# Kernel tuning notes

Hardware: AMD Instinct MI355X
Metric: run time of the kernel (lower is better)

## Reference

```python
import jax, jax.numpy as jnp
import numpy as np

B = 1      # batch
D = 64     # octree grid side at this level
N = 65536  # active voxels
C = 32     # channels (nin == nout for resblock)
K = 3      # kernel size


def _offsets():
    r = jnp.arange(K) - K // 2
    oz, oy, ox = jnp.meshgrid(r, r, r, indexing='ij')
    return jnp.stack([oz.ravel(), oy.ravel(), ox.ravel()], axis=-1)  # [27,3] (kz,ky,kx order)


def octree_conv3d(values, indices, mask_values, kernel, bias, activation=None):
    # values: [N,Cin], indices: [N,4] (b,z,y,x), mask_values: [N,1]
    Cin = values.shape[-1]
    Cout = kernel.shape[-1]
    taps = kernel.reshape(K * K * K, Cin, Cout)            # kz,ky,kx order == kernel[kz,ky,kx]
    vals = jnp.einsum('nc,tcd->tnd', values, taps)         # [27,N,Cout]
    offs = _offsets()                                      # [27,3]
    coords = indices[:, 1:]                                # [N,3]
    # shift = [0, kz-1, ky-1, kx-1]; clamp to [0, D-1] (stride=inv_stride=1)
    sh = jnp.clip(coords[None, :, :] + offs[:, None, :], 0, D - 1)  # [27,N,3]
    lin = indices[:, 0][None, :] * (D * D * D) + sh[..., 0] * (D * D) + sh[..., 1] * D + sh[..., 2]
    grid = jnp.zeros((B * D * D * D, Cout), dtype=values.dtype)
    grid = grid.at[lin.reshape(-1)].add(vals.reshape(-1, Cout))     # scatter-add == coalesce sum
    out_lin = indices[:, 0] * (D * D * D) + coords[:, 0] * (D * D) + coords[:, 1] * D + coords[:, 2]
    gathered = grid[out_lin]                               # [N,Cout] values at mask positions
    out = (gathered + mask_values * bias[None, :]) * mask_values     # result + mask*bias; result*mask
    if activation is not None:
        out = activation(out)
    return out


def setup_inputs() -> dict:
    key = jax.random.key(0)
    k1, k2, k3, k4, k5, k6 = jax.random.split(key, 6)
    G = B * D * D * D
    perm = jax.random.permutation(k1, G)[:N]               # unique (coalesced) voxel indices
    b = perm // (D * D * D)
    rem = perm % (D * D * D)
    z = rem // (D * D)
    y = (rem // D) % D
    x = rem % D
    indices = jnp.stack([b, z, y, x], axis=-1).astype(jnp.int64)   # [N,4]
    values = jax.random.normal(k2, (N, C), dtype=jnp.float32)
    mask_values = jnp.ones((N, 1), dtype=jnp.float32)
    stdv = 1.0 / np.sqrt(K * K * K * C)
    kern1 = (jax.random.uniform(k3, (K, K, K, C, C)) - 0.5) * 2.0 * stdv
    bias1 = (jax.random.uniform(k4, (C,)) - 0.5) * 2.0 * stdv
    kern2 = (jax.random.uniform(k5, (K, K, K, C, C)) - 0.5) * 2.0 * stdv
    bias2 = (jax.random.uniform(k6, (C,)) - 0.5) * 2.0 * stdv
    return {'values': values, 'indices': indices, 'mask_values': mask_values,
            'kern1': kern1, 'bias1': bias1, 'kern2': kern2, 'bias2': bias2}


def reference(values, indices, mask_values, kern1, bias1, kern2, bias2):
    # OctreeResblock: conv(relu) -> conv -> residual add, all on the sparse index set
    h = octree_conv3d(values, indices, mask_values, kern1, bias1, activation=jax.nn.relu)
    h = octree_conv3d(h, indices, mask_values, kern2, bias2, activation=None)
    return values + h
```

## Files before the change

### kernel.cpp

```cpp
#include <hip/hip_runtime.h>

#define NPTS 65536
#define CCH  32
#define DDIM 64
#define GVOX (DDIM*DDIM*DDIM)
#define MAXTILES 4128

typedef _Float16 half8  __attribute__((ext_vector_type(8)));
typedef _Float16 half4v __attribute__((ext_vector_type(4)));
typedef float    floatx4 __attribute__((ext_vector_type(4)));

__global__ __launch_bounds__(256) void k_prep0(
    int* __restrict__ map, int* __restrict__ sorted,
    const float* __restrict__ values, _Float16* __restrict__ valsh,
    const float* __restrict__ k1, const float* __restrict__ k2,
    _Float16* __restrict__ w1, _Float16* __restrict__ w2,
    _Float16* __restrict__ hh, int* __restrict__ pcoord,
    int* __restrict__ cnt, int* __restrict__ slot)
{
  int tid = blockIdx.x * 256 + threadIdx.x;
  if (tid < GVOX/4) { ((int4*)map)[tid] = make_int4(-1,-1,-1,-1); return; }
  tid -= GVOX/4;
  if (tid < MAXTILES*16) { sorted[tid] = NPTS; return; }
  tid -= MAXTILES*16;
  if (tid < (NPTS*CCH)/4) {
    float4 v = ((const float4*)values)[tid];
    half4v h = { (_Float16)v.x, (_Float16)v.y, (_Float16)v.z, (_Float16)v.w };
    ((half4v*)valsh)[tid] = h; return;
  }
  tid -= (NPTS*CCH)/4;
  if (tid < 27*CCH*CCH) {
    int t = tid/(CCH*CCH), r = tid%(CCH*CCH);
    int cin = r/CCH, cout = r%CCH;
    int o = (t*CCH + cout)*CCH + cin;
    w1[o] = (_Float16)k1[tid]; w2[o] = (_Float16)k2[tid]; return;
  }
  tid -= 27*CCH*CCH;
  if (tid < CCH) { valsh[NPTS*CCH+tid] = (_Float16)0.f; hh[NPTS*CCH+tid] = (_Float16)0.f; return; }
  tid -= CCH;
  if (tid < 27) { cnt[tid] = 0; slot[tid] = 0; return; }
  tid -= 27;
  if (tid == 0) pcoord[NPTS] = 0;
}
#define PREP0_THREADS (GVOX/4 + MAXTILES*16 + (NPTS*CCH)/4 + 27*CCH*CCH + CCH + 27 + 1)

__global__ __launch_bounds__(256) void k_prep1(const int* __restrict__ idx,
                                               int* __restrict__ map,
                                               int* __restrict__ pcoord,
                                               int* __restrict__ cls,
                                               int* __restrict__ cnt)
{
  __shared__ int lcnt[27];
  if (threadIdx.x < 27) lcnt[threadIdx.x] = 0;
  __syncthreads();
  const int n = blockIdx.x*256 + threadIdx.x;
  const int b = idx[4*n], z = idx[4*n+1], y = idx[4*n+2], x = idx[4*n+3];
  map[((b*DDIM + z)*DDIM + y)*DDIM + x] = n;
  pcoord[n] = (b<<18) | (z<<12) | (y<<6) | x;
  const int cz = (z==0)?0:((z==DDIM-1)?2:1);
  const int cy = (y==0)?0:((y==DDIM-1)?2:1);
  const int cx = (x==0)?0:((x==DDIM-1)?2:1);
  const int c = cz*9 + cy*3 + cx;
  cls[n] = c;
  atomicAdd(&lcnt[c], 1);
  __syncthreads();
  if (threadIdx.x < 27 && lcnt[threadIdx.x]) atomicAdd(&cnt[threadIdx.x], lcnt[threadIdx.x]);
}

__global__ void k_prep2(const int* __restrict__ cnt, int* __restrict__ clsbase,
                        int* __restrict__ tstart, int* __restrict__ ntiles)
{
  if (threadIdx.x == 0 && blockIdx.x == 0) {
    int b = 0, tb = 0;
    for (int c = 0; c < 27; ++c) {
      clsbase[c] = b; tstart[c] = tb;
      int nt = (cnt[c] + 15) >> 4;
      b += nt << 4; tb += nt;
    }
    tstart[27] = tb; *ntiles = tb;
  }
}

__global__ __launch_bounds__(256) void k_prep3(const int* __restrict__ cls,
                                               const int* __restrict__ clsbase,
                                               int* __restrict__ slot,
                                               int* __restrict__ sorted,
                                               const int* __restrict__ tstart,
                                               const int* __restrict__ ntp,
                                               int* __restrict__ tileclass)
{
  if (blockIdx.x < NPTS/256) {
    __shared__ int lcnt[27], lbase[27];
    if (threadIdx.x < 27) lcnt[threadIdx.x] = 0;
    __syncthreads();
    const int n = blockIdx.x*256 + threadIdx.x;
    const int c = cls[n];
    const int lrank = atomicAdd(&lcnt[c], 1);
    __syncthreads();
    if (threadIdx.x < 27)
      lbase[threadIdx.x] = lcnt[threadIdx.x] ? atomicAdd(&slot[threadIdx.x], lcnt[threadIdx.x]) : 0;
    __syncthreads();
    sorted[clsbase[c] + lbase[c] + lrank] = n;
  } else {
    const int i = (blockIdx.x - NPTS/256)*256 + threadIdx.x;
    if (i >= MAXTILES) return;
    const int nt = *ntp;
    int c = 13;
    if (i < nt) {
      for (int cc = 0; cc < 27; ++cc)
        if (i >= tstart[cc] && i < tstart[cc+1]) { c = cc; break; }
    }
    tileclass[i] = c;
  }
}

template<int MODE>
__global__ __launch_bounds__(256) void conv_mfma(
    const _Float16* __restrict__ A,
    const int* __restrict__ map,
    const int* __restrict__ pcoord,
    const int* __restrict__ sorted,
    const int* __restrict__ tileclass,
    const int* __restrict__ ntp,
    const _Float16* __restrict__ WT,
    const float* __restrict__ bias,
    const float* __restrict__ mask,
    const float* __restrict__ resid,
    _Float16* __restrict__ hout,
    float* __restrict__ fout)
{
  const int tile = blockIdx.x*4 + (threadIdx.x >> 6);
  if (tile >= *ntp) return;
  const int lane = threadIdx.x & 63;
  const int m = lane & 15, quad = lane >> 4;
  const int scls = __builtin_amdgcn_readfirstlane(tileclass[tile]);
  const int cz = scls/9, cy = (scls/3)%3, cx = scls%3;

  const int pid = sorted[tile*16 + m];
  const int pc  = pcoord[pid];
  const int bb = pc>>18, z = (pc>>12)&63, y = (pc>>6)&63, x = pc&63;
  const int linb = bb << 18;
  const int az[3] = { max(z-1,0)<<12, z<<12, min(z+1,DDIM-1)<<12 };
  const int ay[3] = { max(y-1,0)<<6,  y<<6,  min(y+1,DDIM-1)<<6 };
  const int ax[3] = { max(x-1,0),     x,     min(x+1,DDIM-1) };

  floatx4 acc0 = {0.f,0.f,0.f,0.f};
  floatx4 acc1 = {0.f,0.f,0.f,0.f};

#pragma unroll
  for (int j = 0; j < 27; ++j) {
    const int jz = j/9, jy = (j/3)%3, jx = j%3;
    const int tz = (cz==1) ? (2-jz) : ((jz==1) ? 1 : ((cz==0) ? 0 : 2));
    const int ty = (cy==1) ? (2-jy) : ((jy==1) ? 1 : ((cy==0) ? 0 : 2));
    const int tx = (cx==1) ? (2-jx) : ((jx==1) ? 1 : ((cx==0) ? 0 : 2));
    const int t  = tz*9 + ty*3 + tx;
    int src = map[linb | az[jz] | ay[jy] | ax[jx]];
    src = (src < 0) ? NPTS : src;
    half8 a  = *(const half8*)(A + src*CCH + quad*8);
    const _Float16* wr = WT + t*(CCH*CCH);
    half8 b0 = *(const half8*)(wr + m*CCH + quad*8);
    half8 b1 = *(const half8*)(wr + (16+m)*CCH + quad*8);
    acc0 = __builtin_amdgcn_mfma_f32_16x16x32_f16(a, b0, acc0, 0, 0, 0);
    acc1 = __builtin_amdgcn_mfma_f32_16x16x32_f16(a, b1, acc1, 0, 0, 0);
  }

  const float bi0 = bias[m], bi1 = bias[m+16];
#pragma unroll
  for (int reg = 0; reg < 4; ++reg) {
    const int r  = quad*4 + reg;
    const int pr = sorted[tile*16 + r];
    if (pr >= NPTS) continue;
    const float mk = mask[pr];
    float v0 = (acc0[reg] + mk*bi0) * mk;
    float v1 = (acc1[reg] + mk*bi1) * mk;
    if (MODE == 0) {
      v0 = fmaxf(v0, 0.f); v1 = fmaxf(v1, 0.f);
      hout[pr*CCH + m]      = (_Float16)v0;
      hout[pr*CCH + m + 16] = (_Float16)v1;
    } else {
      fout[pr*CCH + m]      = resid[pr*CCH + m]      + v0;
      fout[pr*CCH + m + 16] = resid[pr*CCH + m + 16] + v1;
    }
  }
}


extern "C" void kernel_launch(void* const* d_in, const int* in_sizes, int n_in,
                              void* d_out, int out_size, void* d_ws, size_t ws_size,
                              hipStream_t stream) {
  const float* values = (const float*)d_in[0];
  const int*   indices= (const int*)  d_in[1];
  const float* maskv  = (const float*)d_in[2];
  const float* kern1  = (const float*)d_in[3];
  const float* bias1  = (const float*)d_in[4];
  const float* kern2  = (const float*)d_in[5];
  const float* bias2  = (const float*)d_in[6];
  float* out = (float*)d_out;

  char* ws = (char*)d_ws;
  size_t off = 0;
  auto alloc = [&](size_t bytes) { void* p = ws + off; off = (off + bytes + 255) & ~(size_t)255; return p; };
  int*      map      = (int*)     alloc(GVOX*4);
  int*      pcoord   = (int*)     alloc((NPTS+1)*4);
  int*      cls      = (int*)     alloc(NPTS*4);
  int*      sorted   = (int*)     alloc(MAXTILES*16*4);
  int*      tileclass= (int*)     alloc(MAXTILES*4);
  int*      cnt      = (int*)     alloc(27*4);
  int*      slot     = (int*)     alloc(27*4);
  int*      clsbase  = (int*)     alloc(27*4);
  int*      tstart   = (int*)     alloc(28*4);
  int*      ntiles   = (int*)     alloc(4);
  _Float16* valsh    = (_Float16*)alloc((NPTS+1)*CCH*2);
  _Float16* hh       = (_Float16*)alloc((NPTS+1)*CCH*2);
  _Float16* wt1      = (_Float16*)alloc(27*CCH*CCH*2);
  _Float16* wt2      = (_Float16*)alloc(27*CCH*CCH*2);

  k_prep0<<<(PREP0_THREADS + 255)/256, 256, 0, stream>>>(
      map, sorted, values, valsh, kern1, kern2, wt1, wt2, hh, pcoord, cnt, slot);
  k_prep1<<<NPTS/256, 256, 0, stream>>>(indices, map, pcoord, cls, cnt);
  k_prep2<<<1, 64, 0, stream>>>(cnt, clsbase, tstart, ntiles);
  k_prep3<<<NPTS/256 + (MAXTILES+255)/256, 256, 0, stream>>>(
      cls, clsbase, slot, sorted, tstart, ntiles, tileclass);

  conv_mfma<0><<<MAXTILES/4, 256, 0, stream>>>(valsh, map, pcoord, sorted, tileclass,
                                               ntiles, wt1, bias1, maskv, nullptr, hh, nullptr);
  conv_mfma<1><<<MAXTILES/4, 256, 0, stream>>>(hh, map, pcoord, sorted, tileclass,
                                               ntiles, wt2, bias2, maskv, values, nullptr, out);
}
```

Measured before the change: 148.5 us.

## Use 32-row MFMA tiles with LDS-staged weights and precomputed neighbor table

Tiles grow from 16 to 32 points and use the 32x32x16 MFMA, with one 32-column accumulator replacing two 16x16 ones. All 27 weight taps are copied once per block into LDS in a fragment-friendly layout. A new kernel builds the 27-entry neighbor index table once, so both convolutions share it instead of each repeating the hash-map lookups. In exchange there is an extra launch, a 54KB LDS footprint that may cap occupancy, a per-block weight copy, and extra global traffic to write and read the neighbor table.

```diff
diff --git a/kernel.cpp b/kernel.cpp
--- a/kernel.cpp
+++ b/kernel.cpp
@@ -4,11 +4,11 @@
 #define CCH  32
 #define DDIM 64
 #define GVOX (DDIM*DDIM*DDIM)
-#define MAXTILES 4128
-
-typedef _Float16 half8  __attribute__((ext_vector_type(8)));
-typedef _Float16 half4v __attribute__((ext_vector_type(4)));
-typedef float    floatx4 __attribute__((ext_vector_type(4)));
+#define MAXT 2080
+
+typedef _Float16 half8   __attribute__((ext_vector_type(8)));
+typedef _Float16 half4v  __attribute__((ext_vector_type(4)));
+typedef float    floatx16 __attribute__((ext_vector_type(16)));
 
 __global__ __launch_bounds__(256) void k_prep0(
     int* __restrict__ map, int* __restrict__ sorted,
@@ -21,8 +21,8 @@
   int tid = blockIdx.x * 256 + threadIdx.x;
   if (tid < GVOX/4) { ((int4*)map)[tid] = make_int4(-1,-1,-1,-1); return; }
   tid -= GVOX/4;
-  if (tid < MAXTILES*16) { sorted[tid] = NPTS; return; }
-  tid -= MAXTILES*16;
+  if (tid < MAXT*32/4) { ((int4*)sorted)[tid] = make_int4(NPTS,NPTS,NPTS,NPTS); return; }
+  tid -= MAXT*32/4;
   if (tid < (NPTS*CCH)/4) {
     float4 v = ((const float4*)values)[tid];
     half4v h = { (_Float16)v.x, (_Float16)v.y, (_Float16)v.z, (_Float16)v.w };
@@ -32,8 +32,9 @@
   if (tid < 27*CCH*CCH) {
     int t = tid/(CCH*CCH), r = tid%(CCH*CCH);
     int cin = r/CCH, cout = r%CCH;
-    int o = (t*CCH + cout)*CCH + cin;
-    w1[o] = (_Float16)k1[tid]; w2[o] = (_Float16)k2[tid]; return;
+    int h = cin >> 4, kq = (cin >> 3) & 1, j = cin & 7;
+    int dst = t*1024 + h*512 + (kq*32 + cout)*8 + j;
+    w1[dst] = (_Float16)k1[tid]; w2[dst] = (_Float16)k2[tid]; return;
   }
   tid -= 27*CCH*CCH;
   if (tid < CCH) { valsh[NPTS*CCH+tid] = (_Float16)0.f; hh[NPTS*CCH+tid] = (_Float16)0.f; return; }
@@ -42,7 +43,7 @@
   tid -= 27;
   if (tid == 0) pcoord[NPTS] = 0;
 }
-#define PREP0_THREADS (GVOX/4 + MAXTILES*16 + (NPTS*CCH)/4 + 27*CCH*CCH + CCH + 27 + 1)
+#define PREP0_THREADS (GVOX/4 + MAXT*32/4 + (NPTS*CCH)/4 + 27*CCH*CCH + CCH + 27 + 1)
 
 __global__ __launch_bounds__(256) void k_prep1(const int* __restrict__ idx,
                                                int* __restrict__ map,
@@ -74,8 +75,8 @@
     int b = 0, tb = 0;
     for (int c = 0; c < 27; ++c) {
       clsbase[c] = b; tstart[c] = tb;
-      int nt = (cnt[c] + 15) >> 4;
-      b += nt << 4; tb += nt;
+      int nt = (cnt[c] + 31) >> 5;
+      b += nt << 5; tb += nt;
     }
     tstart[27] = tb; *ntiles = tb;
   }
@@ -103,7 +104,7 @@
     sorted[clsbase[c] + lbase[c] + lrank] = n;
   } else {
     const int i = (blockIdx.x - NPTS/256)*256 + threadIdx.x;
-    if (i >= MAXTILES) return;
+    if (i >= MAXT) return;
     const int nt = *ntp;
     int c = 13;
     if (i < nt) {
@@ -114,39 +115,66 @@
   }
 }
 
-template<int MODE>
-__global__ __launch_bounds__(256) void conv_mfma(
-    const _Float16* __restrict__ A,
-    const int* __restrict__ map,
-    const int* __restrict__ pcoord,
-    const int* __restrict__ sorted,
-    const int* __restrict__ tileclass,
-    const int* __restrict__ ntp,
-    const _Float16* __restrict__ WT,
-    const float* __restrict__ bias,
-    const float* __restrict__ mask,
-    const float* __restrict__ resid,
-    _Float16* __restrict__ hout,
-    float* __restrict__ fout)
-{
-  const int tile = blockIdx.x*4 + (threadIdx.x >> 6);
-  if (tile >= *ntp) return;
-  const int lane = threadIdx.x & 63;
-  const int m = lane & 15, quad = lane >> 4;
-  const int scls = __builtin_amdgcn_readfirstlane(tileclass[tile]);
-  const int cz = scls/9, cy = (scls/3)%3, cx = scls%3;
-
-  const int pid = sorted[tile*16 + m];
+__global__ __launch_bounds__(256) void k_nbr(const int* __restrict__ sorted,
+                                             const int* __restrict__ pcoord,
+                                             const int* __restrict__ map,
+                                             int* __restrict__ nbr)
+{
+  const int i = blockIdx.x*256 + threadIdx.x;
+  if (i >= MAXT*32) return;
+  const int tile = i >> 5, m = i & 31;
+  const int pid = sorted[i];
   const int pc  = pcoord[pid];
   const int bb = pc>>18, z = (pc>>12)&63, y = (pc>>6)&63, x = pc&63;
   const int linb = bb << 18;
   const int az[3] = { max(z-1,0)<<12, z<<12, min(z+1,DDIM-1)<<12 };
   const int ay[3] = { max(y-1,0)<<6,  y<<6,  min(y+1,DDIM-1)<<6 };
   const int ax[3] = { max(x-1,0),     x,     min(x+1,DDIM-1) };
-
-  floatx4 acc0 = {0.f,0.f,0.f,0.f};
-  floatx4 acc1 = {0.f,0.f,0.f,0.f};
-
+#pragma unroll
+  for (int j = 0; j < 27; ++j) {
+    int src = map[linb | az[j/9] | ay[(j/3)%3] | ax[j%3]];
+    nbr[(tile*27 + j)*32 + m] = (src < 0) ? NPTS : src;
+  }
+}
+
+template<int MODE>
+__global__ __launch_bounds__(256) void conv32(
+    const _Float16* __restrict__ A,
+    const int* __restrict__ sorted,
+    const int* __restrict__ tileclass,
+    const int* __restrict__ nbr,
+    const int* __restrict__ ntp,
+    const _Float16* __restrict__ wfrag,
+    const float* __restrict__ bias,
+    const float* __restrict__ mask,
+    const float* __restrict__ resid,
+    _Float16* __restrict__ hout,
+    float* __restrict__ fout)
+{
+  __shared__ _Float16 bs[27*1024];
+  {
+    const int4* s = (const int4*)wfrag;
+    int4* d = (int4*)bs;
+#pragma unroll
+    for (int i = 0; i < 14; ++i) {
+      const int o = threadIdx.x + i*256;
+      if (o < 27*1024/8) d[o] = s[o];
+    }
+  }
+  __syncthreads();
+
+  const int tile = blockIdx.x*4 + (threadIdx.x >> 6);
+  if (tile >= *ntp) return;
+  const int lane = threadIdx.x & 63;
+  const int m = lane & 31, kh = lane >> 5;
+  const int scls = __builtin_amdgcn_readfirstlane(tileclass[tile]);
+  const int cz = scls/9, cy = (scls/3)%3, cx = scls%3;
+
+  int nb[27];
+#pragma unroll
+  for (int j = 0; j < 27; ++j) nb[j] = nbr[(tile*27 + j)*32 + m];
+
+  floatx16 acc = {};
 #pragma unroll
   for (int j = 0; j < 27; ++j) {
     const int jz = j/9, jy = (j/3)%3, jx = j%3;
@@ -154,33 +182,26 @@
     const int ty = (cy==1) ? (2-jy) : ((jy==1) ? 1 : ((cy==0) ? 0 : 2));
     const int tx = (cx==1) ? (2-jx) : ((jx==1) ? 1 : ((cx==0) ? 0 : 2));
     const int t  = tz*9 + ty*3 + tx;
-    int src = map[linb | az[jz] | ay[jy] | ax[jx]];
-    src = (src < 0) ? NPTS : src;
-    half8 a  = *(const half8*)(A + src*CCH + quad*8);
-    const _Float16* wr = WT + t*(CCH*CCH);
-    half8 b0 = *(const half8*)(wr + m*CCH + quad*8);
-    half8 b1 = *(const half8*)(wr + (16+m)*CCH + quad*8);
-    acc0 = __builtin_amdgcn_mfma_f32_16x16x32_f16(a, b0, acc0, 0, 0, 0);
-    acc1 = __builtin_amdgcn_mfma_f32_16x16x32_f16(a, b1, acc1, 0, 0, 0);
-  }
-
-  const float bi0 = bias[m], bi1 = bias[m+16];
-#pragma unroll
-  for (int reg = 0; reg < 4; ++reg) {
-    const int r  = quad*4 + reg;
-    const int pr = sorted[tile*16 + r];
+    const _Float16* ap = A + nb[j]*CCH + kh*8;
+    half8 alo = *(const half8*)ap;
+    half8 ahi = *(const half8*)(ap + 16);
+    const _Float16* bp = bs + t*1024 + lane*8;
+    half8 blo = *(const half8*)bp;
+    half8 bhi = *(const half8*)(bp + 512);
+    acc = __builtin_amdgcn_mfma_f32_32x32x16_f16(alo, blo, acc, 0, 0, 0);
+    acc = __builtin_amdgcn_mfma_f32_32x32x16_f16(ahi, bhi, acc, 0, 0, 0);
+  }
+
+  const float bi = bias[m];
+#pragma unroll
+  for (int r = 0; r < 16; ++r) {
+    const int row = (r&3) + 8*(r>>2) + 4*kh;
+    const int pr  = sorted[tile*32 + row];
     if (pr >= NPTS) continue;
     const float mk = mask[pr];
-    float v0 = (acc0[reg] + mk*bi0) * mk;
-    float v1 = (acc1[reg] + mk*bi1) * mk;
-    if (MODE == 0) {
-      v0 = fmaxf(v0, 0.f); v1 = fmaxf(v1, 0.f);
-      hout[pr*CCH + m]      = (_Float16)v0;
-      hout[pr*CCH + m + 16] = (_Float16)v1;
-    } else {
-      fout[pr*CCH + m]      = resid[pr*CCH + m]      + v0;
-      fout[pr*CCH + m + 16] = resid[pr*CCH + m + 16] + v1;
-    }
+    const float v = (acc[r] + mk*bi) * mk;
+    if (MODE == 0) hout[pr*CCH + m] = (_Float16)fmaxf(v, 0.f);
+    else           fout[pr*CCH + m] = resid[pr*CCH + m] + v;
   }
 }
 
@@ -203,8 +224,9 @@
   int*      map      = (int*)     alloc(GVOX*4);
   int*      pcoord   = (int*)     alloc((NPTS+1)*4);
   int*      cls      = (int*)     alloc(NPTS*4);
-  int*      sorted   = (int*)     alloc(MAXTILES*16*4);
-  int*      tileclass= (int*)     alloc(MAXTILES*4);
+  int*      sorted   = (int*)     alloc(MAXT*32*4);
+  int*      tileclass= (int*)     alloc(MAXT*4);
+  int*      nbr      = (int*)     alloc((size_t)MAXT*27*32*4);
   int*      cnt      = (int*)     alloc(27*4);
   int*      slot     = (int*)     alloc(27*4);
   int*      clsbase  = (int*)     alloc(27*4);
@@ -212,18 +234,19 @@
   int*      ntiles   = (int*)     alloc(4);
   _Float16* valsh    = (_Float16*)alloc((NPTS+1)*CCH*2);
   _Float16* hh       = (_Float16*)alloc((NPTS+1)*CCH*2);
-  _Float16* wt1      = (_Float16*)alloc(27*CCH*CCH*2);
-  _Float16* wt2      = (_Float16*)alloc(27*CCH*CCH*2);
+  _Float16* wf1      = (_Float16*)alloc(27*1024*2);
+  _Float16* wf2      = (_Float16*)alloc(27*1024*2);
 
   k_prep0<<<(PREP0_THREADS + 255)/256, 256, 0, stream>>>(
-      map, sorted, values, valsh, kern1, kern2, wt1, wt2, hh, pcoord, cnt, slot);
+      map, sorted, values, valsh, kern1, kern2, wf1, wf2, hh, pcoord, cnt, slot);
   k_prep1<<<NPTS/256, 256, 0, stream>>>(indices, map, pcoord, cls, cnt);
   k_prep2<<<1, 64, 0, stream>>>(cnt, clsbase, tstart, ntiles);
-  k_prep3<<<NPTS/256 + (MAXTILES+255)/256, 256, 0, stream>>>(
+  k_prep3<<<NPTS/256 + (MAXT+255)/256, 256, 0, stream>>>(
       cls, clsbase, slot, sorted, tstart, ntiles, tileclass);
-
-  conv_mfma<0><<<MAXTILES/4, 256, 0, stream>>>(valsh, map, pcoord, sorted, tileclass,
-                                               ntiles, wt1, bias1, maskv, nullptr, hh, nullptr);
-  conv_mfma<1><<<MAXTILES/4, 256, 0, stream>>>(hh, map, pcoord, sorted, tileclass,
-                                               ntiles, wt2, bias2, maskv, values, nullptr, out);
-}
+  k_nbr  <<<(MAXT*32)/256, 256, 0, stream>>>(sorted, pcoord, map, nbr);
+
+  conv32<0><<<MAXT/4, 256, 0, stream>>>(valsh, sorted, tileclass, nbr, ntiles,
+                                        wf1, bias1, maskv, nullptr, hh, nullptr);
+  conv32<1><<<MAXT/4, 256, 0, stream>>>(hh, sorted, tileclass, nbr, ntiles,
+                                        wf2, bias2, maskv, values, nullptr, out);
+}
```

Result: slower. 151.9 us (+2.3%).
